# Kernel tuning notes

Measured on AMD Instinct MI355X. Metric: run time of the kernel, lower is better.

The kernel has to match this reference:

```python
import jax, jax.numpy as jnp
import numpy as np

C_IN, C_OUT, K = 64, 64, 3
KK = K * K


def _conv3x3(x, w, b):
    # x: [B, Cin, H, W], w: [Cout, Cin, 3, 3], b: [Cout] or None. stride 1, pad 1.
    y = jax.lax.conv_general_dilated(
        x, w, window_strides=(1, 1), padding=((1, 1), (1, 1)),
        dimension_numbers=("NCHW", "OIHW", "NCHW"))
    if b is not None:
        y = y + b[None, :, None, None]
    return y


def _deform_conv2d(x, offset, mask, weight):
    # torchvision.ops.deform_conv2d with stride=1, pad=1, dilation=1, 1 offset group.
    # x: [B,C,H,W]; offset: [B,2*KK,H,W] (per-tap (dy,dx)); mask: [B,KK,H,W];
    # weight: [O,C,K,K]
    B, C, H, W = x.shape
    O = weight.shape[0]
    ky, kx = jnp.meshgrid(jnp.arange(K), jnp.arange(K), indexing="ij")
    hs = jnp.arange(H)
    ws = jnp.arange(W)
    # base sample positions per tap k=(ky*K+kx): [KK,H,W]
    base_y = (hs[:, None] - 1)[None] + ky.reshape(KK, 1, 1)
    base_x = (ws[None, :] - 1)[None] + kx.reshape(KK, 1, 1)
    off = offset.reshape(B, KK, 2, H, W)
    py = base_y[None].astype(x.dtype) + off[:, :, 0]  # [B,KK,H,W]
    px = base_x[None].astype(x.dtype) + off[:, :, 1]

    y0 = jnp.floor(py)
    x0 = jnp.floor(px)
    wy = py - y0  # bilinear fractional weights
    wx = px - x0
    y0i = y0.astype(jnp.int32)
    x0i = x0.astype(jnp.int32)

    imflat = x.reshape(B, C, H * W)

    def gather_b(im, idx):  # im: [C,HW], idx: [KK,H,W] -> [C,KK,H,W]
        return im[:, idx]

    val = jnp.zeros((B, C, KK, H, W), x.dtype)
    for dy, dx in ((0, 0), (0, 1), (1, 0), (1, 1)):
        yc = y0i + dy
        xc = x0i + dx
        valid = ((yc >= 0) & (yc < H) & (xc >= 0) & (xc < W)).astype(x.dtype)
        cw = (wy if dy else (1.0 - wy)) * (wx if dx else (1.0 - wx)) * valid
        idx = jnp.clip(yc, 0, H - 1) * W + jnp.clip(xc, 0, W - 1)
        g = jax.vmap(gather_b)(imflat, idx)  # [B,C,KK,H,W]
        val = val + cw[:, None] * g
    val = val * mask[:, None]  # modulation
    # contract 9-tap patches with conv weight
    return jnp.einsum("bckhw,ock->bohw", val, weight.reshape(O, C, KK))


def setup_inputs() -> dict:
    key = jax.random.key(0)
    ks = jax.random.split(key, 8)
    B, H, W = 4, 96, 96
    cin2 = 2 * C_IN + 2
    frame_i = jax.random.normal(ks[0], (B, C_IN, H, W), jnp.float32)
    frame_j = jax.random.normal(ks[1], (B, C_IN, H, W), jnp.float32)
    flow_ij = jax.random.normal(ks[2], (B, 2, H, W), jnp.float32)
    # small random weights so offsets are nonzero (zero-init would degenerate)
    w_off = jax.random.normal(ks[3], (2 * KK, cin2, K, K), jnp.float32) * 0.01
    b_off = jax.random.normal(ks[4], (2 * KK,), jnp.float32) * 0.1
    w_mod = jax.random.normal(ks[5], (KK, cin2, K, K), jnp.float32) * 0.01
    b_mod = jax.random.normal(ks[6], (KK,), jnp.float32) * 0.1
    w_reg = jax.random.normal(ks[7], (C_OUT, C_IN, K, K), jnp.float32) * (1.0 / np.sqrt(C_IN * KK))
    return {"frame_i": frame_i, "frame_j": frame_j, "flow_ij": flow_ij,
            "w_off": w_off, "b_off": b_off, "w_mod": w_mod, "b_mod": b_mod,
            "w_reg": w_reg}


def reference(frame_i, frame_j, flow_ij, w_off, b_off, w_mod, b_mod, w_reg):
    offset_input = jnp.concatenate([frame_i, frame_j, flow_ij], axis=1)
    offset = _conv3x3(offset_input, w_off, b_off)            # [B,2*KK,H,W]
    modulator = 2.0 * jax.nn.sigmoid(_conv3x3(offset_input, w_mod, b_mod))  # [B,KK,H,W]
    return _deform_conv2d(frame_j, offset, modulator, w_reg)
```

## Files before the change

kernel.cpp:

```cpp
#include <hip/hip_runtime.h>
#include <math.h>

#define BB   4
#define HH   96
#define WW   96
#define HW   (HH * WW)
#define CIN  64
#define COUT 64
#define C2B  192
#define NROW (BB * HW)
#define ZROW NROW
#define NSTRIP (NROW / 16)
#define BPX3 (NSTRIP / 8)
#define NA   (9 * 5 * 2 * 512)
#define NW   (9 * 2 * 4 * 512)
#define PXB2 (NROW / 32)
#define PWBLK 324
#define TSX  35
#define RS   20
#define PR   55

typedef short v8s __attribute__((ext_vector_type(8)));
typedef float v4f __attribute__((ext_vector_type(4)));

__device__ __forceinline__ unsigned short f2bf(float f) {
    unsigned u = __float_as_uint(f);
    return (unsigned short)((u + 0x7FFFu + ((u >> 16) & 1u)) >> 16);
}
__device__ __forceinline__ unsigned pack2(float a, float b) {
    return (unsigned)f2bf(a) | ((unsigned)f2bf(b) << 16);
}
__device__ __forceinline__ unsigned bil2(unsigned a, unsigned b, unsigned c,
                                         unsigned d, float w00, float w01,
                                         float w10, float w11) {
    float lo = w00 * __uint_as_float(a << 16) + w01 * __uint_as_float(b << 16)
             + w10 * __uint_as_float(c << 16) + w11 * __uint_as_float(d << 16);
    float hi = w00 * __uint_as_float(a & 0xffff0000u)
             + w01 * __uint_as_float(b & 0xffff0000u)
             + w10 * __uint_as_float(c & 0xffff0000u)
             + w11 * __uint_as_float(d & 0xffff0000u);
    return pack2(lo, hi);
}

__global__ __launch_bounds__(256) void prep_kernel(
    const float* __restrict__ fi, const float* __restrict__ fj,
    const float* __restrict__ fl, const float* __restrict__ w_off,
    const float* __restrict__ w_mod, const float* __restrict__ w_reg,
    unsigned short* __restrict__ xt, unsigned short* __restrict__ wa2f,
    unsigned short* __restrict__ wb2f)
{
    int blk = blockIdx.x;
    if (blk < PXB2) {
        __shared__ __align__(16) unsigned tile[64 * TSX];
        int tid = threadIdx.x;
        int p = tid & 63, cg = tid >> 6;
        int u = blk >> 1, half = blk & 1;
        int r0 = u * 64;
        int b = r0 / HW;
        int hw = r0 - b * HW + p;
        uint4* dst = (uint4*)(xt + (size_t)r0 * C2B);
        if (half == 0) {
            const float* pi = fi + (size_t)b * CIN * HW + hw;
#pragma unroll
            for (int d = 0; d < 8; ++d) {
                int c = cg * 16 + 2 * d;
                tile[p * TSX + cg * 8 + d] =
                    pack2(pi[(size_t)c * HW], pi[(size_t)(c + 1) * HW]);
            }
            __syncthreads();
#pragma unroll
            for (int i = 0; i < 2; ++i) {
                int gq = i * 256 + tid;
                int rl = gq >> 3, c4 = gq & 7;
                const unsigned* s = &tile[rl * TSX + c4 * 4];
                uint4 v = {s[0], s[1], s[2], s[3]};
                dst[rl * 24 + c4] = v;
            }
        } else {
            const float* pj = fj + (size_t)b * CIN * HW + hw;
#pragma unroll
            for (int d = 0; d < 8; ++d) {
                int c = cg * 16 + 2 * d;
                tile[p * TSX + cg * 8 + d] =
                    pack2(pj[(size_t)c * HW], pj[(size_t)(c + 1) * HW]);
            }
            if (cg == 0) {
                const float* pf = fl + (size_t)b * 2 * HW + hw;
                tile[p * TSX + 32] = pack2(pf[0], pf[HW]);
            }
            __syncthreads();
#pragma unroll
            for (int i = 0; i < 4; ++i) {
                int gq = i * 256 + tid;
                int rl = gq >> 4, c4 = gq & 15;
                uint4 v = {0u, 0u, 0u, 0u};
                if (c4 < 8) {
                    const unsigned* s = &tile[rl * TSX + c4 * 4];
                    v.x = s[0]; v.y = s[1]; v.z = s[2]; v.w = s[3];
                } else if (c4 == 8) {
                    v.x = tile[rl * TSX + 32];
                }
                int pc4 = (c4 < 8) ? ((c4 & 3) * 2 + (c4 >> 2)) : c4;
                dst[rl * 24 + 8 + pc4] = v;
            }
        }
    } else if (blk < PXB2 + PWBLK) {
        int e = (blk - PXB2) * 256 + threadIdx.x;
        if (e < NA) {
            int t  = e / 5120;
            int r1 = e - t * 5120;
            int ks = r1 >> 10;
            int r2 = r1 & 1023;
            int nt = r2 >> 9;
            int l9 = r2 & 511;
            int l  = l9 >> 3, ee = l9 & 7;
            int m  = l & 15, g = l >> 4;
            int oc = nt * 16 + m;
            int ch = ks * 32 + g * 8 + ee;
            float v = 0.0f;
            if (oc < 27 && ch < 130) {
                if (oc < 18) v = w_off[((size_t)oc * 130 + ch) * 9 + t];
                else         v = w_mod[((size_t)(oc - 18) * 130 + ch) * 9 + t];
            }
            wa2f[e] = f2bf(v);
        } else {
            int e2 = e - NA;
            if (e2 < NW) {
                int k  = e2 >> 12;
                int r1 = e2 & 4095;
                int ks = r1 >> 11;
                int r2 = r1 & 2047;
                int nt = r2 >> 9;
                int l9 = r2 & 511;
                int l  = l9 >> 3, ee = l9 & 7;
                int m  = l & 15, g = l >> 4;
                int o  = nt * 16 + m;
                int c  = ks * 32 + g * 8 + ee;
                wb2f[e2] = f2bf(w_reg[((size_t)o * 64 + c) * 9 + k]);
            }
        }
    } else {
        if (threadIdx.x < 24) {
            uint4 z = {0u, 0u, 0u, 0u};
            ((uint4*)(xt + (size_t)ZROW * C2B))[threadIdx.x] = z;
        }
    }
}

__global__ __launch_bounds__(256, 2) void fused_kernel(
    const unsigned short* __restrict__ xt,
    const unsigned short* __restrict__ wa2f,
    const unsigned short* __restrict__ wb2f,
    const float* __restrict__ b_off, const float* __restrict__ b_mod,
    float* __restrict__ out)
{
    __shared__ __align__(16) uint4 patch4[20 * PR];
    __shared__ float lraw[16 * 28];
    __shared__ __align__(16) float red[4][64 * RS];

    int l = threadIdx.x & 63;
    int wid = __builtin_amdgcn_readfirstlane(threadIdx.x >> 6);
    int m = l & 15, g = l >> 4;
    int strip = (blockIdx.x & 7) * BPX3 + (blockIdx.x >> 3);
    int b = strip / (HW / 16);
    int hw0 = (strip - b * (HW / 16)) * 16;
    int hw = hw0 + m;
    int x = hw % WW, y = hw / WW;
    int y0b = hw0 / WW, x0b = hw0 - y0b * WW;
    int t0 = wid * 2;
    int ntap = (wid == 3) ? 3 : 2;

#pragma unroll
    for (int i = 0; i < 5; ++i) {
        int item = i * 256 + threadIdx.x;
        if (item < 1080) {
            int run = item / 360;
            int rem = item - run * 360;
            int r18 = rem / 20;
            int c8  = rem - r18 * 20;
            int yy = y0b + run - 1;
            int xx = x0b - 1 + r18;
            bool ok = ((unsigned)yy < HH) && ((unsigned)xx < WW);
            uint4 v = {0u, 0u, 0u, 0u};
            if (ok)
                v = ((const uint4*)(xt + (size_t)(b * HW + yy * WW + xx) * C2B))[c8];
            patch4[c8 * PR + run * 18 + r18] = v;
        }
    }
    __syncthreads();

    v4f acc0 = {0.f, 0.f, 0.f, 0.f};
    v4f acc1 = {0.f, 0.f, 0.f, 0.f};
#pragma unroll
    for (int ti = 0; ti < 3; ++ti) {
        if (ti < ntap) {
            int t = t0 + ti;
            int r = (t / 3) * 18 + (t % 3) + m;
#pragma unroll
            for (int ks = 0; ks < 5; ++ks) {
                int c8 = (ks == 0) ? g : (ks == 1) ? 4 + g
                       : (ks == 2) ? 8 + 2 * g : (ks == 3) ? 9 + 2 * g : 16 + g;
                v8s a = *(const v8s*)&patch4[c8 * PR + r];
                const unsigned short* wp =
                    wa2f + ((size_t)((t * 5 + ks) * 2)) * 512 + l * 8;
                v8s b0 = *(const v8s*)(wp);
                v8s b1 = *(const v8s*)(wp + 512);
                acc0 = __builtin_amdgcn_mfma_f32_16x16x32_bf16(a, b0, acc0, 0, 0, 0);
                acc1 = __builtin_amdgcn_mfma_f32_16x16x32_bf16(a, b1, acc1, 0, 0, 0);
            }
        }
    }

    if (wid != 0) {
        float* rb = &red[wid][l * RS];
        *(v4f*)(rb + 0) = acc0;
        *(v4f*)(rb + 4) = acc1;
    }
    __syncthreads();
    if (wid == 0) {
#pragma unroll
        for (int sw = 1; sw < 4; ++sw) {
            const float* rb = &red[sw][l * RS];
            acc0 += *(const v4f*)(rb + 0);
            acc1 += *(const v4f*)(rb + 4);
        }
        float v0[4] = {acc0.x, acc0.y, acc0.z, acc0.w};
        float v1[4] = {acc1.x, acc1.y, acc1.z, acc1.w};
        float bo0 = b_off[m];
        int oc1 = 16 + m;
#pragma unroll
        for (int r = 0; r < 4; ++r)
            lraw[(g * 4 + r) * 28 + m] = v0[r] + bo0;
        if (oc1 < 18) {
            float bo1 = b_off[oc1];
#pragma unroll
            for (int r = 0; r < 4; ++r)
                lraw[(g * 4 + r) * 28 + oc1] = v1[r] + bo1;
        } else if (oc1 < 27) {
            float bm = b_mod[oc1 - 18];
#pragma unroll
            for (int r = 0; r < 4; ++r)
                lraw[(g * 4 + r) * 28 + oc1] =
                    2.0f / (1.0f + expf(-(v1[r] + bm)));
        }
    }
    __syncthreads();

    float cw[3][4];
    uint4 gbuf[3][8];
#pragma unroll
    for (int ti = 0; ti < 3; ++ti) {
        if (ti < ntap) {
            int k = t0 + ti;
            int ky = k / 3, kx = k - 3 * ky;
            float dy = lraw[m * 28 + 2 * k];
            float dx = lraw[m * 28 + 2 * k + 1];
            float mm = lraw[m * 28 + 18 + k];

            float py = (float)(y - 1 + ky) + dy;
            float px = (float)(x - 1 + kx) + dx;
            float fy = floorf(py), fx = floorf(px);
            int   y0 = (int)fy,    x0 = (int)fx;
            float wy = py - fy,    wx = px - fx;
            int   y1 = y0 + 1,     x1 = x0 + 1;

            bool y0v = (y0 >= 0) && (y0 < HH);
            bool y1v = (y1 >= 0) && (y1 < HH);
            bool x0v = (x0 >= 0) && (x0 < WW);
            bool x1v = (x1 >= 0) && (x1 < WW);

            cw[ti][0] = (1.f - wy) * (1.f - wx) * ((y0v && x0v) ? mm : 0.f);
            cw[ti][1] = (1.f - wy) * wx         * ((y0v && x1v) ? mm : 0.f);
            cw[ti][2] = wy * (1.f - wx)         * ((y1v && x0v) ? mm : 0.f);
            cw[ti][3] = wy * wx                 * ((y1v && x1v) ? mm : 0.f);

            int y0c = min(max(y0, 0), HH - 1), y1c = min(max(y1, 0), HH - 1);
            int x0c = min(max(x0, 0), WW - 1), x1c = min(max(x1, 0), WW - 1);
            int rb = b * HW;
            const unsigned short* r00 = xt + (size_t)(rb + y0c * WW + x0c) * C2B + 64 + g * 16;
            const unsigned short* r01 = xt + (size_t)(rb + y0c * WW + x1c) * C2B + 64 + g * 16;
            const unsigned short* r10 = xt + (size_t)(rb + y1c * WW + x0c) * C2B + 64 + g * 16;
            const unsigned short* r11 = xt + (size_t)(rb + y1c * WW + x1c) * C2B + 64 + g * 16;
#pragma unroll
            for (int ks = 0; ks < 2; ++ks) {
                gbuf[ti][ks * 4 + 0] = *(const uint4*)(r00 + ks * 8);
                gbuf[ti][ks * 4 + 1] = *(const uint4*)(r01 + ks * 8);
                gbuf[ti][ks * 4 + 2] = *(const uint4*)(r10 + ks * 8);
                gbuf[ti][ks * 4 + 3] = *(const uint4*)(r11 + ks * 8);
            }
        }
    }
    __builtin_amdgcn_sched_barrier(0);

    v4f acc[4];
#pragma unroll
    for (int nt = 0; nt < 4; ++nt) acc[nt] = (v4f){0.f, 0.f, 0.f, 0.f};

#pragma unroll
    for (int ti = 0; ti < 3; ++ti) {
        if (ti < ntap) {
            int k = t0 + ti;
            float w00 = cw[ti][0], w01 = cw[ti][1];
            float w10 = cw[ti][2], w11 = cw[ti][3];
            v8s afrag[2];
#pragma unroll
            for (int ks = 0; ks < 2; ++ks) {
                uint4 u00 = gbuf[ti][ks * 4 + 0];
                uint4 u01 = gbuf[ti][ks * 4 + 1];
                uint4 u10 = gbuf[ti][ks * 4 + 2];
                uint4 u11 = gbuf[ti][ks * 4 + 3];
                uint4 ov;
                ov.x = bil2(u00.x, u01.x, u10.x, u11.x, w00, w01, w10, w11);
                ov.y = bil2(u00.y, u01.y, u10.y, u11.y, w00, w01, w10, w11);
                ov.z = bil2(u00.z, u01.z, u10.z, u11.z, w00, w01, w10, w11);
                ov.w = bil2(u00.w, u01.w, u10.w, u11.w, w00, w01, w10, w11);
                afrag[ks] = __builtin_bit_cast(v8s, ov);
            }
#pragma unroll
            for (int nt = 0; nt < 4; ++nt) {
#pragma unroll
                for (int ks = 0; ks < 2; ++ks) {
                    const unsigned short* wp =
                        wb2f + ((size_t)((k * 2 + ks) * 4 + nt)) * 512 + l * 8;
                    v8s bb = *(const v8s*)wp;
                    acc[nt] = __builtin_amdgcn_mfma_f32_16x16x32_bf16(
                        afrag[ks], bb, acc[nt], 0, 0, 0);
                }
            }
        }
    }

    {
        float* rb = &red[wid][l * RS];
        *(v4f*)(rb + 0)  = acc[0];
        *(v4f*)(rb + 4)  = acc[1];
        *(v4f*)(rb + 8)  = acc[2];
        *(v4f*)(rb + 12) = acc[3];
    }
    __syncthreads();
    {
        v4f s = {0.f, 0.f, 0.f, 0.f};
#pragma unroll
        for (int sw = 0; sw < 4; ++sw)
            s += *(const v4f*)(&red[sw][l * RS + wid * 4]);
        float* op = out + ((size_t)(b * COUT + wid * 16 + m)) * HW + hw0 + g * 4;
        *(v4f*)op = s;
    }
}

extern "C" void kernel_launch(void* const* d_in, const int* in_sizes, int n_in,
                              void* d_out, int out_size, void* d_ws, size_t ws_size,
                              hipStream_t stream)
{
    const float* frame_i = (const float*)d_in[0];
    const float* frame_j = (const float*)d_in[1];
    const float* flow_ij = (const float*)d_in[2];
    const float* w_off   = (const float*)d_in[3];
    const float* b_off   = (const float*)d_in[4];
    const float* w_mod   = (const float*)d_in[5];
    const float* b_mod   = (const float*)d_in[6];
    const float* w_reg   = (const float*)d_in[7];
    float* out = (float*)d_out;

    unsigned short* xt   = (unsigned short*)d_ws;
    unsigned short* wa2f = xt + (size_t)(NROW + 1) * C2B;
    unsigned short* wb2f = wa2f + NA;

    prep_kernel<<<PXB2 + PWBLK + 1, 256, 0, stream>>>(
        frame_i, frame_j, flow_ij, w_off, w_mod, w_reg, xt, wa2f, wb2f);

    fused_kernel<<<NSTRIP, 256, 0, stream>>>(
        xt, wa2f, wb2f, b_off, b_mod, out);
}
```

Measured before the change: 127.1 us.

## Alias shared buffers, drop gather prefetch registers, raise occupancy target to five

Shared memory now sits in one pool: the patch buffer is reused for the final cross-wave reduction and the offset scratch sits at its tail, which cuts LDS per block. The first reduction is split across all four waves instead of wave 0, and uses the faster __expf intrinsic. The deformable gather loads and their MFMAs are now done one tap at a time instead of prefetching all taps into registers, and launch bounds ask for five blocks per SM. This trades memory-latency hiding within a wave for more resident waves, and the reduction layout changes from vector to scalar LDS accesses.

Result: faster. 123.8 us (-2.6%).

```diff
diff --git a/kernel.cpp b/kernel.cpp
--- a/kernel.cpp
+++ b/kernel.cpp
@@ -17,7 +17,6 @@
 #define PXB2 (NROW / 32)
 #define PWBLK 324
 #define TSX  35
-#define RS   20
 #define PR   55
 
 typedef short v8s __attribute__((ext_vector_type(8)));
@@ -147,16 +146,19 @@
     }
 }
 
-__global__ __launch_bounds__(256, 2) void fused_kernel(
+__global__ __launch_bounds__(256, 5) void fused_kernel(
     const unsigned short* __restrict__ xt,
     const unsigned short* __restrict__ wa2f,
     const unsigned short* __restrict__ wb2f,
     const float* __restrict__ b_off, const float* __restrict__ b_mod,
     float* __restrict__ out)
 {
-    __shared__ __align__(16) uint4 patch4[20 * PR];
-    __shared__ float lraw[16 * 28];
-    __shared__ __align__(16) float red[4][64 * RS];
+    __shared__ __align__(16) unsigned char pool[18176];
+    __shared__ float red1[4][8][64];
+
+    uint4* patch4 = (uint4*)pool;
+    float* red2   = (float*)pool;
+    float* lraw   = (float*)(pool + 16384);
 
     int l = threadIdx.x & 63;
     int wid = __builtin_amdgcn_readfirstlane(threadIdx.x >> 6);
@@ -168,7 +170,6 @@
     int x = hw % WW, y = hw / WW;
     int y0b = hw0 / WW, x0b = hw0 - y0b * WW;
     int t0 = wid * 2;
-    int ntap = (wid == 3) ? 3 : 2;
 
 #pragma unroll
     for (int i = 0; i < 5; ++i) {
@@ -191,158 +192,150 @@
 
     v4f acc0 = {0.f, 0.f, 0.f, 0.f};
     v4f acc1 = {0.f, 0.f, 0.f, 0.f};
-#pragma unroll
-    for (int ti = 0; ti < 3; ++ti) {
-        if (ti < ntap) {
-            int t = t0 + ti;
-            int r = (t / 3) * 18 + (t % 3) + m;
-#pragma unroll
-            for (int ks = 0; ks < 5; ++ks) {
-                int c8 = (ks == 0) ? g : (ks == 1) ? 4 + g
-                       : (ks == 2) ? 8 + 2 * g : (ks == 3) ? 9 + 2 * g : 16 + g;
-                v8s a = *(const v8s*)&patch4[c8 * PR + r];
-                const unsigned short* wp =
-                    wa2f + ((size_t)((t * 5 + ks) * 2)) * 512 + l * 8;
-                v8s b0 = *(const v8s*)(wp);
-                v8s b1 = *(const v8s*)(wp + 512);
-                acc0 = __builtin_amdgcn_mfma_f32_16x16x32_bf16(a, b0, acc0, 0, 0, 0);
-                acc1 = __builtin_amdgcn_mfma_f32_16x16x32_bf16(a, b1, acc1, 0, 0, 0);
-            }
-        }
-    }
-
-    if (wid != 0) {
-        float* rb = &red[wid][l * RS];
-        *(v4f*)(rb + 0) = acc0;
-        *(v4f*)(rb + 4) = acc1;
+    {
+        int ntap = (wid == 3) ? 3 : 2;
+#pragma unroll
+        for (int ti = 0; ti < 3; ++ti) {
+            if (ti < ntap) {
+                int t = t0 + ti;
+                int r = (t / 3) * 18 + (t % 3) + m;
+#pragma unroll
+                for (int ks = 0; ks < 5; ++ks) {
+                    int c8 = (ks == 0) ? g : (ks == 1) ? 4 + g
+                           : (ks == 2) ? 8 + 2 * g : (ks == 3) ? 9 + 2 * g
+                           : 16 + g;
+                    v8s a = *(const v8s*)&patch4[c8 * PR + r];
+                    const unsigned short* wp =
+                        wa2f + ((size_t)((t * 5 + ks) * 2)) * 512 + l * 8;
+                    v8s b0 = *(const v8s*)(wp);
+                    v8s b1 = *(const v8s*)(wp + 512);
+                    acc0 = __builtin_amdgcn_mfma_f32_16x16x32_bf16(a, b0, acc0, 0, 0, 0);
+                    acc1 = __builtin_amdgcn_mfma_f32_16x16x32_bf16(a, b1, acc1, 0, 0, 0);
+                }
+            }
+        }
+    }
+
+    {
+#pragma unroll
+        for (int j = 0; j < 4; ++j) red1[wid][j][l] = acc0[j];
+#pragma unroll
+        for (int j = 0; j < 4; ++j) red1[wid][4 + j][l] = acc1[j];
     }
     __syncthreads();
-    if (wid == 0) {
-#pragma unroll
-        for (int sw = 1; sw < 4; ++sw) {
-            const float* rb = &red[sw][l * RS];
-            acc0 += *(const v4f*)(rb + 0);
-            acc1 += *(const v4f*)(rb + 4);
-        }
-        float v0[4] = {acc0.x, acc0.y, acc0.z, acc0.w};
-        float v1[4] = {acc1.x, acc1.y, acc1.z, acc1.w};
-        float bo0 = b_off[m];
-        int oc1 = 16 + m;
-#pragma unroll
-        for (int r = 0; r < 4; ++r)
-            lraw[(g * 4 + r) * 28 + m] = v0[r] + bo0;
-        if (oc1 < 18) {
-            float bo1 = b_off[oc1];
+
+    {
+#pragma unroll
+        for (int jj = 0; jj < 2; ++jj) {
+            int j = t0 + jj;
+            float v = red1[0][j][l] + red1[1][j][l]
+                    + red1[2][j][l] + red1[3][j][l];
+            int r = j & 3;
+            int oc = (j < 4) ? m : 16 + m;
+            int pos = g * 4 + r;
+            if (oc < 18) {
+                lraw[pos * 28 + oc] = v + b_off[oc];
+            } else if (oc < 27) {
+                lraw[pos * 28 + oc] =
+                    2.0f / (1.0f + __expf(-(v + b_mod[oc - 18])));
+            }
+        }
+    }
+    __syncthreads();
+
+    v4f acc[4];
+#pragma unroll
+    for (int nt = 0; nt < 4; ++nt) acc[nt] = (v4f){0.f, 0.f, 0.f, 0.f};
+
+    const unsigned short* rowb =
+        xt + (size_t)(b * HW) * C2B + 64 + g * 16;
+
+    auto do_tap = [&](int k) {
+        int ky = k / 3, kx = k - 3 * ky;
+        float dy = lraw[m * 28 + 2 * k];
+        float dx = lraw[m * 28 + 2 * k + 1];
+        float mm = lraw[m * 28 + 18 + k];
+
+        float py = (float)(y - 1 + ky) + dy;
+        float px = (float)(x - 1 + kx) + dx;
+        float fy = floorf(py), fx = floorf(px);
+        int   y0 = (int)fy,    x0 = (int)fx;
+        float wy = py - fy,    wx = px - fx;
+        int   y1 = y0 + 1,     x1 = x0 + 1;
+
+        bool y0v = (y0 >= 0) && (y0 < HH);
+        bool y1v = (y1 >= 0) && (y1 < HH);
+        bool x0v = (x0 >= 0) && (x0 < WW);
+        bool x1v = (x1 >= 0) && (x1 < WW);
+
+        float w00 = (1.f - wy) * (1.f - wx) * ((y0v && x0v) ? mm : 0.f);
+        float w01 = (1.f - wy) * wx         * ((y0v && x1v) ? mm : 0.f);
+        float w10 = wy * (1.f - wx)         * ((y1v && x0v) ? mm : 0.f);
+        float w11 = wy * wx                 * ((y1v && x1v) ? mm : 0.f);
+
+        int y0c = min(max(y0, 0), HH - 1), y1c = min(max(y1, 0), HH - 1);
+        int x0c = min(max(x0, 0), WW - 1), x1c = min(max(x1, 0), WW - 1);
+        const unsigned short* r00 = rowb + (size_t)(y0c * WW + x0c) * C2B;
+        const unsigned short* r01 = rowb + (size_t)(y0c * WW + x1c) * C2B;
+        const unsigned short* r10 = rowb + (size_t)(y1c * WW + x0c) * C2B;
+        const unsigned short* r11 = rowb + (size_t)(y1c * WW + x1c) * C2B;
+
+        uint4 a00 = *(const uint4*)(r00);
+        uint4 a01 = *(const uint4*)(r01);
+        uint4 a10 = *(const uint4*)(r10);
+        uint4 a11 = *(const uint4*)(r11);
+        uint4 c00 = *(const uint4*)(r00 + 8);
+        uint4 c01 = *(const uint4*)(r01 + 8);
+        uint4 c10 = *(const uint4*)(r10 + 8);
+        uint4 c11 = *(const uint4*)(r11 + 8);
+
+        uint4 ov0, ov1;
+        ov0.x = bil2(a00.x, a01.x, a10.x, a11.x, w00, w01, w10, w11);
+        ov0.y = bil2(a00.y, a01.y, a10.y, a11.y, w00, w01, w10, w11);
+        ov0.z = bil2(a00.z, a01.z, a10.z, a11.z, w00, w01, w10, w11);
+        ov0.w = bil2(a00.w, a01.w, a10.w, a11.w, w00, w01, w10, w11);
+        ov1.x = bil2(c00.x, c01.x, c10.x, c11.x, w00, w01, w10, w11);
+        ov1.y = bil2(c00.y, c01.y, c10.y, c11.y, w00, w01, w10, w11);
+        ov1.z = bil2(c00.z, c01.z, c10.z, c11.z, w00, w01, w10, w11);
+        ov1.w = bil2(c00.w, c01.w, c10.w, c11.w, w00, w01, w10, w11);
+        v8s af0 = __builtin_bit_cast(v8s, ov0);
+        v8s af1 = __builtin_bit_cast(v8s, ov1);
+
+#pragma unroll
+        for (int nt = 0; nt < 4; ++nt) {
+            const unsigned short* wp0 =
+                wb2f + ((size_t)((k * 2 + 0) * 4 + nt)) * 512 + l * 8;
+            const unsigned short* wp1 =
+                wb2f + ((size_t)((k * 2 + 1) * 4 + nt)) * 512 + l * 8;
+            v8s bb0 = *(const v8s*)wp0;
+            v8s bb1 = *(const v8s*)wp1;
+            acc[nt] = __builtin_amdgcn_mfma_f32_16x16x32_bf16(af0, bb0, acc[nt], 0, 0, 0);
+            acc[nt] = __builtin_amdgcn_mfma_f32_16x16x32_bf16(af1, bb1, acc[nt], 0, 0, 0);
+        }
+    };
+
+    do_tap(t0);
+    do_tap(t0 + 1);
+    if (wid == 3) do_tap(8);
+
+    {
+#pragma unroll
+        for (int nt = 0; nt < 4; ++nt)
 #pragma unroll
             for (int r = 0; r < 4; ++r)
-                lraw[(g * 4 + r) * 28 + oc1] = v1[r] + bo1;
-        } else if (oc1 < 27) {
-            float bm = b_mod[oc1 - 18];
-#pragma unroll
-            for (int r = 0; r < 4; ++r)
-                lraw[(g * 4 + r) * 28 + oc1] =
-                    2.0f / (1.0f + expf(-(v1[r] + bm)));
-        }
+                red2[(wid * 16 + nt * 4 + r) * 64 + l] = acc[nt][r];
     }
     __syncthreads();
-
-    float cw[3][4];
-    uint4 gbuf[3][8];
-#pragma unroll
-    for (int ti = 0; ti < 3; ++ti) {
-        if (ti < ntap) {
-            int k = t0 + ti;
-            int ky = k / 3, kx = k - 3 * ky;
-            float dy = lraw[m * 28 + 2 * k];
-            float dx = lraw[m * 28 + 2 * k + 1];
-            float mm = lraw[m * 28 + 18 + k];
-
-            float py = (float)(y - 1 + ky) + dy;
-            float px = (float)(x - 1 + kx) + dx;
-            float fy = floorf(py), fx = floorf(px);
-            int   y0 = (int)fy,    x0 = (int)fx;
-            float wy = py - fy,    wx = px - fx;
-            int   y1 = y0 + 1,     x1 = x0 + 1;
-
-            bool y0v = (y0 >= 0) && (y0 < HH);
-            bool y1v = (y1 >= 0) && (y1 < HH);
-            bool x0v = (x0 >= 0) && (x0 < WW);
-            bool x1v = (x1 >= 0) && (x1 < WW);
-
-            cw[ti][0] = (1.f - wy) * (1.f - wx) * ((y0v && x0v) ? mm : 0.f);
-            cw[ti][1] = (1.f - wy) * wx         * ((y0v && x1v) ? mm : 0.f);
-            cw[ti][2] = wy * (1.f - wx)         * ((y1v && x0v) ? mm : 0.f);
-            cw[ti][3] = wy * wx                 * ((y1v && x1v) ? mm : 0.f);
-
-            int y0c = min(max(y0, 0), HH - 1), y1c = min(max(y1, 0), HH - 1);
-            int x0c = min(max(x0, 0), WW - 1), x1c = min(max(x1, 0), WW - 1);
-            int rb = b * HW;
-            const unsigned short* r00 = xt + (size_t)(rb + y0c * WW + x0c) * C2B + 64 + g * 16;
-            const unsigned short* r01 = xt + (size_t)(rb + y0c * WW + x1c) * C2B + 64 + g * 16;
-            const unsigned short* r10 = xt + (size_t)(rb + y1c * WW + x0c) * C2B + 64 + g * 16;
-            const unsigned short* r11 = xt + (size_t)(rb + y1c * WW + x1c) * C2B + 64 + g * 16;
-#pragma unroll
-            for (int ks = 0; ks < 2; ++ks) {
-                gbuf[ti][ks * 4 + 0] = *(const uint4*)(r00 + ks * 8);
-                gbuf[ti][ks * 4 + 1] = *(const uint4*)(r01 + ks * 8);
-                gbuf[ti][ks * 4 + 2] = *(const uint4*)(r10 + ks * 8);
-                gbuf[ti][ks * 4 + 3] = *(const uint4*)(r11 + ks * 8);
-            }
-        }
-    }
-    __builtin_amdgcn_sched_barrier(0);
-
-    v4f acc[4];
-#pragma unroll
-    for (int nt = 0; nt < 4; ++nt) acc[nt] = (v4f){0.f, 0.f, 0.f, 0.f};
-
-#pragma unroll
-    for (int ti = 0; ti < 3; ++ti) {
-        if (ti < ntap) {
-            int k = t0 + ti;
-            float w00 = cw[ti][0], w01 = cw[ti][1];
-            float w10 = cw[ti][2], w11 = cw[ti][3];
-            v8s afrag[2];
-#pragma unroll
-            for (int ks = 0; ks < 2; ++ks) {
-                uint4 u00 = gbuf[ti][ks * 4 + 0];
-                uint4 u01 = gbuf[ti][ks * 4 + 1];
-                uint4 u10 = gbuf[ti][ks * 4 + 2];
-                uint4 u11 = gbuf[ti][ks * 4 + 3];
-                uint4 ov;
-                ov.x = bil2(u00.x, u01.x, u10.x, u11.x, w00, w01, w10, w11);
-                ov.y = bil2(u00.y, u01.y, u10.y, u11.y, w00, w01, w10, w11);
-                ov.z = bil2(u00.z, u01.z, u10.z, u11.z, w00, w01, w10, w11);
-                ov.w = bil2(u00.w, u01.w, u10.w, u11.w, w00, w01, w10, w11);
-                afrag[ks] = __builtin_bit_cast(v8s, ov);
-            }
-#pragma unroll
-            for (int nt = 0; nt < 4; ++nt) {
-#pragma unroll
-                for (int ks = 0; ks < 2; ++ks) {
-                    const unsigned short* wp =
-                        wb2f + ((size_t)((k * 2 + ks) * 4 + nt)) * 512 + l * 8;
-                    v8s bb = *(const v8s*)wp;
-                    acc[nt] = __builtin_amdgcn_mfma_f32_16x16x32_bf16(
-                        afrag[ks], bb, acc[nt], 0, 0, 0);
-                }
-            }
-        }
-    }
-
-    {
-        float* rb = &red[wid][l * RS];
-        *(v4f*)(rb + 0)  = acc[0];
-        *(v4f*)(rb + 4)  = acc[1];
-        *(v4f*)(rb + 8)  = acc[2];
-        *(v4f*)(rb + 12) = acc[3];
-    }
-    __syncthreads();
     {
         v4f s = {0.f, 0.f, 0.f, 0.f};
 #pragma unroll
-        for (int sw = 0; sw < 4; ++sw)
-            s += *(const v4f*)(&red[sw][l * RS + wid * 4]);
+        for (int r = 0; r < 4; ++r) {
+            float t = 0.f;
+#pragma unroll
+            for (int sw = 0; sw < 4; ++sw)
+                t += red2[(sw * 16 + wid * 4 + r) * 64 + l];
+            s[r] = t;
+        }
         float* op = out + ((size_t)(b * COUT + wid * 16 + m)) * HW + hw0 + g * 4;
         *(v4f*)op = s;
     }
```
